# Performance work log

Hardware: AMD Instinct MI355X
Metric: run time of the kernel (lower is better)

## Reference

```python
import jax, jax.numpy as jnp
import numpy as np

N = 100000
E = 1600000
D_PCA = 50
D_BIO = 64
HID = 32
HEADS = 4
OUT = 50
EPS = 1e-5


def setup_inputs() -> dict:
    key = jax.random.key(0)
    ks = jax.random.split(key, 32)
    g = lambda i, shape, s=0.05: jax.random.normal(ks[i], shape, dtype=jnp.float32) * s
    inp = {
        'x_pca': jax.random.normal(ks[0], (N, D_PCA), dtype=jnp.float32),
        'x_bio': jax.random.normal(ks[1], (N, D_BIO), dtype=jnp.float32),
        'edge_index': jax.random.randint(ks[2], (2, E), 0, N, dtype=jnp.int32),
        # bio encoder: Linear(64,16) -> BN(16) -> ELU -> Linear(16,16) -> ELU
        'bioW1': g(3, (16, D_BIO)), 'biob1': g(4, (16,)),
        'bn0_g': 1.0 + g(5, (16,)), 'bn0_b': g(6, (16,)),
        'bn0_m': g(7, (16,)), 'bn0_v': 1.0 + 0.1 * jax.random.uniform(ks[8], (16,), dtype=jnp.float32),
        'bioW2': g(9, (16, 16)), 'biob2': g(10, (16,)),
        # GATv2 layer 1: in = 50+16 = 66, out = HEADS*HID concat
        'Wl1': g(11, (HEADS * HID, D_PCA + 16)), 'bl1': g(12, (HEADS * HID,)),
        'Wr1': g(13, (HEADS * HID, D_PCA + 16)), 'br1': g(14, (HEADS * HID,)),
        'att1': g(15, (HEADS, HID)), 'bias1': g(16, (HEADS * HID,)),
        'bn1_g': 1.0 + g(17, (HEADS * HID,)), 'bn1_b': g(18, (HEADS * HID,)),
        'bn1_m': g(19, (HEADS * HID,)), 'bn1_v': 1.0 + 0.1 * jax.random.uniform(ks[20], (HEADS * HID,), dtype=jnp.float32),
        # GATv2 layer 2: in = HEADS*HID, heads=1, concat=False
        'Wl2': g(21, (HID, HEADS * HID)), 'bl2': g(22, (HID,)),
        'Wr2': g(23, (HID, HEADS * HID)), 'br2': g(24, (HID,)),
        'att2': g(25, (1, HID)), 'bias2': g(26, (HID,)),
        'bn2_g': 1.0 + g(27, (HID,)), 'bn2_b': g(28, (HID,)),
        'bn2_m': g(29, (HID,)), 'bn2_v': 1.0 + 0.1 * jax.random.uniform(ks[30], (HID,), dtype=jnp.float32),
        'predW': g(31, (OUT, HID)), 'predb': jnp.zeros((OUT,), dtype=jnp.float32),
    }
    return inp


def _bn(h, gm, bt, mean, var):
    # BatchNorm1d in eval mode (running stats)
    return (h - mean) * jax.lax.rsqrt(var + EPS) * gm + bt


def _gatv2(x, src, dst, Wl, bl, Wr, br, att, bias, heads, out_dim, concat):
    n = x.shape[0]
    xl = (x @ Wl.T + bl).reshape(n, heads, out_dim)  # source transform
    xr = (x @ Wr.T + br).reshape(n, heads, out_dim)  # target transform
    e = jax.nn.leaky_relu(xl[src] + xr[dst], 0.2)    # [E,H,C]
    logits = jnp.einsum('ehc,hc->eh', e, att)        # [E,H]
    m = jax.ops.segment_max(logits, dst, num_segments=n)
    a = jnp.exp(logits - m[dst])
    denom = jax.ops.segment_sum(a, dst, num_segments=n)
    alpha = a / (denom[dst] + 1e-16)                 # segment softmax over dst
    out = jax.ops.segment_sum(xl[src] * alpha[..., None], dst, num_segments=n)
    out = out.reshape(n, heads * out_dim) if concat else out.mean(axis=1)
    return out + bias


def reference(x_pca, x_bio, edge_index,
              bioW1, biob1, bn0_g, bn0_b, bn0_m, bn0_v, bioW2, biob2,
              Wl1, bl1, Wr1, br1, att1, bias1, bn1_g, bn1_b, bn1_m, bn1_v,
              Wl2, bl2, Wr2, br2, att2, bias2, bn2_g, bn2_b, bn2_m, bn2_v,
              predW, predb):
    n = x_pca.shape[0]
    # add self-loops (PyG GATv2Conv default)
    loop = jnp.arange(n, dtype=edge_index.dtype)
    src = jnp.concatenate([edge_index[0], loop])
    dst = jnp.concatenate([edge_index[1], loop])

    # bio encoder
    h_bio = jax.nn.elu(_bn(x_bio @ bioW1.T + biob1, bn0_g, bn0_b, bn0_m, bn0_v))
    h_bio = jax.nn.elu(h_bio @ bioW2.T + biob2)
    x = jnp.concatenate([x_pca, h_bio], axis=1)  # [N, 66]

    h = _gatv2(x, src, dst, Wl1, bl1, Wr1, br1, att1, bias1, HEADS, HID, True)
    h = jax.nn.elu(_bn(h, bn1_g, bn1_b, bn1_m, bn1_v))  # dropout off (eval)
    h = _gatv2(h, src, dst, Wl2, bl2, Wr2, br2, att2, bias2, 1, HID, False)
    h = jax.nn.elu(_bn(h, bn2_g, bn2_b, bn2_m, bn2_v))
    return h @ predW.T + predb
```

## Files before the change

kernel.cpp:

```cpp
#include <hip/hip_runtime.h>
#include <hip/hip_fp16.h>
#include <cstdint>
#include <cstddef>

#define NN 100000
#define NE 1600000
#define NEP (NE + NN)
#define NBLK 200
#define CHUNK ((NEP + NBLK - 1) / NBLK)
#define NBUCK2 ((NN + 255) / 256)
#define HISTN (NBUCK2 * NBLK)
#define HSCAN_BLOCKS ((HISTN + 1023) / 1024)

typedef __attribute__((ext_vector_type(8))) _Float16 half8;
typedef __attribute__((ext_vector_type(4))) _Float16 h4v;
typedef __attribute__((ext_vector_type(2))) _Float16 h2v;
typedef __attribute__((ext_vector_type(4))) float float4v;

__device__ __forceinline__ float elu_f(float x) {
    return x > 0.f ? x : __expf(x) - 1.f;
}

__device__ __forceinline__ float ex2(float x) {
#if __has_builtin(__builtin_amdgcn_exp2f)
    return __builtin_amdgcn_exp2f(x);
#else
    return exp2f(x);
#endif
}

template<int CTRL>
__device__ __forceinline__ float dpp_add(float x) {
    int s = __builtin_amdgcn_update_dpp(0, __float_as_int(x), CTRL, 0xF, 0xF, true);
    return x + __int_as_float(s);
}
__device__ __forceinline__ float sum4_all(float x) {
    x = dpp_add<0xB1>(x); x = dpp_add<0x4E>(x);
    return x;
}
__device__ __forceinline__ float sum8_all(float x) {
    x = dpp_add<0xB1>(x); x = dpp_add<0x4E>(x); x = dpp_add<0x141>(x);
    return x;
}

__device__ __forceinline__ float dot2f(h2v a, h2v b, float c) {
#if __has_builtin(__builtin_amdgcn_fdot2)
    return __builtin_amdgcn_fdot2(a, b, c, false);
#else
    return fmaf((float)a[0], (float)b[0], fmaf((float)a[1], (float)b[1], c));
#endif
}

__device__ __forceinline__ h2v hmax2v(h2v a, h2v b) {
#if __has_builtin(__builtin_elementwise_max)
    return __builtin_elementwise_max(a, b);
#else
    __half2 r = __hmax2(*(__half2*)&a, *(__half2*)&b);
    return *(h2v*)&r;
#endif
}


__global__ __launch_bounds__(256) void part_hist(const int* __restrict__ ei, int* __restrict__ hist)
{
    __shared__ int cnt[NBUCK2];
    int tid = threadIdx.x, k = blockIdx.x;
    for (int i = tid; i < NBUCK2; i += 256) cnt[i] = 0;
    __syncthreads();
    int e0 = k * CHUNK, e1 = min(e0 + CHUNK, NEP);
    for (int e = e0 + tid; e < e1; e += 256) {
        int dst = (e < NE) ? ei[NE + e] : e - NE;
        atomicAdd(&cnt[dst >> 8], 1);
    }
    __syncthreads();
    for (int i = tid; i < NBUCK2; i += 256) hist[i * NBLK + k] = cnt[i];
}

__global__ __launch_bounds__(256) void scan_p1(const int* __restrict__ src, int* __restrict__ part, int n)
{
    __shared__ int wsum[4];
    int t = threadIdx.x;
    int i0 = blockIdx.x * 1024 + t * 4;
    int s = 0;
    if (i0 + 3 < n) { int4 d = *(const int4*)(src + i0); s = d.x + d.y + d.z + d.w; }
    else { for (int k = 0; k < 4; k++) if (i0 + k < n) s += src[i0 + k]; }
    for (int d = 1; d < 64; d <<= 1) s += __shfl_xor(s, d, 64);
    if ((t & 63) == 0) wsum[t >> 6] = s;
    __syncthreads();
    if (t == 0) part[blockIdx.x] = wsum[0] + wsum[1] + wsum[2] + wsum[3];
}

__global__ __launch_bounds__(128) void scan_p2(int* __restrict__ part, int nb, int* __restrict__ off)
{
    __shared__ int wt[2];
    int t = threadIdx.x;
    int lane = t & 63, w = t >> 6;
    int v = (t < nb) ? part[t] : 0;
    int x = v;
    for (int d = 1; d < 64; d <<= 1) { int y = __shfl_up(x, d, 64); if (lane >= d) x += y; }
    if (lane == 63) wt[w] = x;
    __syncthreads();
    int base = (w == 1) ? wt[0] : 0;
    int excl = base + x - v;
    if (t < nb) part[t] = excl;
    if (t == 0) off[NN] = NEP;
}

__global__ __launch_bounds__(256) void scan_p3(int* __restrict__ data, const int* __restrict__ part, int n)
{
    __shared__ int wsum[4];
    int t = threadIdx.x, lane = t & 63, w = t >> 6;
    int i0 = blockIdx.x * 1024 + t * 4;
    int d0 = 0, d1 = 0, d2 = 0, d3 = 0;
    if (i0 + 3 < n) { int4 d = *(const int4*)(data + i0); d0 = d.x; d1 = d.y; d2 = d.z; d3 = d.w; }
    else if (i0 < n) {
        d0 = data[i0];
        if (i0 + 1 < n) d1 = data[i0 + 1];
        if (i0 + 2 < n) d2 = data[i0 + 2];
    }
    int s = d0 + d1 + d2 + d3;
    int x = s;
    for (int d = 1; d < 64; d <<= 1) { int y = __shfl_up(x, d, 64); if (lane >= d) x += y; }
    if (lane == 63) wsum[w] = x;
    __syncthreads();
    int wb = 0;
    for (int i = 0; i < w; i++) wb += wsum[i];
    int base = part[blockIdx.x] + wb + x - s;
    if (i0 < n)     data[i0]     = base;
    if (i0 + 1 < n) data[i0 + 1] = base + d0;
    if (i0 + 2 < n) data[i0 + 2] = base + d0 + d1;
    if (i0 + 3 < n) data[i0 + 3] = base + d0 + d1 + d2;
}

__global__ __launch_bounds__(256) void part_scatter(const int* __restrict__ ei,
                                                    const int* __restrict__ hist,
                                                    unsigned* __restrict__ ebuf)
{
    __shared__ int cur[NBUCK2];
    int tid = threadIdx.x, k = blockIdx.x;
    for (int i = tid; i < NBUCK2; i += 256) cur[i] = hist[i * NBLK + k];
    __syncthreads();
    int e0 = k * CHUNK, e1 = min(e0 + CHUNK, NEP);
    for (int e = e0 + tid; e < e1; e += 256) {
        int src, dst;
        if (e < NE) { src = ei[e]; dst = ei[NE + e]; } else { src = dst = e - NE; }
        int pos = atomicAdd(&cur[dst >> 8], 1);
        ebuf[pos] = (unsigned)src | ((unsigned)(dst & 255) << 24);
    }
}

__global__ __launch_bounds__(256) void bucket_csr(const int* __restrict__ hist,
                                                  const unsigned* __restrict__ ebuf,
                                                  int* __restrict__ off, int* __restrict__ csr)
{
    __shared__ int cnt[256];
    __shared__ int cur[256];
    __shared__ int wsum[4];
    int b = blockIdx.x;
    int d0 = b << 8;
    int tid = threadIdx.x;
    int e0 = hist[b * NBLK];
    int e1 = (b + 1 < NBUCK2) ? hist[(b + 1) * NBLK] : NEP;
    cnt[tid] = 0;
    __syncthreads();
    for (int i = e0 + tid; i < e1; i += 256) atomicAdd(&cnt[ebuf[i] >> 24], 1);
    __syncthreads();
    int c = cnt[tid];
    int x = c;
    int lane = tid & 63, w = tid >> 6;
    for (int d = 1; d < 64; d <<= 1) { int y = __shfl_up(x, d, 64); if (lane >= d) x += y; }
    if (lane == 63) wsum[w] = x;
    __syncthreads();
    int wb = 0;
    for (int i = 0; i < w; i++) wb += wsum[i];
    int excl = wb + x - c;
    cur[tid] = e0 + excl;
    int node = d0 + tid;
    if (node < NN) off[node] = e0 + excl;
    __syncthreads();
    for (int i = e0 + tid; i < e1; i += 256) {
        unsigned v = ebuf[i];
        int p = atomicAdd(&cur[v >> 24], 1);
        csr[p] = (int)(v & 0xFFFFFF);
    }
}


__global__ __launch_bounds__(256) void bio_kernel(
    const float* __restrict__ xb, const float* __restrict__ xp,
    const float* __restrict__ W1, const float* __restrict__ b1,
    const float* __restrict__ g0, const float* __restrict__ bb0,
    const float* __restrict__ m0, const float* __restrict__ v0,
    const float* __restrict__ W2, const float* __restrict__ b2,
    __half* __restrict__ xh)
{
    __shared__ float sW1[16*64], sW2[16*16], sb1[16], sb2[16], ss[16], st[16];
    int tid = threadIdx.x;
    for (int idx = tid; idx < 1024; idx += 256) sW1[idx] = W1[idx];
    if (tid < 256) sW2[tid] = W2[tid];
    if (tid < 16) {
        sb1[tid] = b1[tid]; sb2[tid] = b2[tid];
        float s = g0[tid] * rsqrtf(v0[tid] + 1e-5f);
        ss[tid] = s; st[tid] = bb0[tid] - m0[tid] * s;
    }
    __syncthreads();
    int i = blockIdx.x * 256 + tid;
    if (i >= NN) return;
    float bio[64];
    const float4* p = (const float4*)(xb + (size_t)i * 64);
    #pragma unroll
    for (int q = 0; q < 16; q++) {
        float4 f = p[q];
        bio[q*4] = f.x; bio[q*4+1] = f.y; bio[q*4+2] = f.z; bio[q*4+3] = f.w;
    }
    float t1[16];
    #pragma unroll
    for (int j = 0; j < 16; j++) {
        float acc = sb1[j];
        #pragma unroll
        for (int k = 0; k < 64; k++) acc += bio[k] * sW1[j*64 + k];
        acc = acc * ss[j] + st[j];
        t1[j] = elu_f(acc);
    }
    __half* xrow = xh + (size_t)i * 96;
    const float* xpr = xp + (size_t)i * 50;
    #pragma unroll
    for (int j = 0; j < 25; j++) {
        float2 f = *(const float2*)(xpr + 2 * j);
        *(__half2*)(xrow + 2 * j) = __floats2half2_rn(f.x, f.y);
    }
    #pragma unroll
    for (int j = 0; j < 16; j++) {
        float acc = sb2[j];
        #pragma unroll
        for (int k = 0; k < 16; k++) acc += t1[k] * sW2[j*16 + k];
        xrow[50 + j] = __float2half(elu_f(acc));
    }
    __half2 z2 = __floats2half2_rn(0.f, 0.f);
    #pragma unroll
    for (int j = 0; j < 15; j++) *(__half2*)(xrow + 66 + 2 * j) = z2;
}


__global__ __launch_bounds__(256) void wconvert_all(
    const float* __restrict__ Wl1, const float* __restrict__ Wr1,
    const float* __restrict__ bl1, const float* __restrict__ br1,
    const float* __restrict__ Wl2, const float* __restrict__ Wr2,
    const float* __restrict__ bl2, const float* __restrict__ br2,
    const float* __restrict__ predW, const float* __restrict__ predb,
    const float* __restrict__ bias1, const float* __restrict__ bn1g,
    const float* __restrict__ bn1b, const float* __restrict__ bn1m,
    const float* __restrict__ bn1v,
    const float* __restrict__ bias2, const float* __restrict__ bn2g,
    const float* __restrict__ bn2b, const float* __restrict__ bn2m,
    const float* __restrict__ bn2v,
    __half* __restrict__ wcat1, float* __restrict__ bcat1,
    __half* __restrict__ wcat2, float* __restrict__ bcat2,
    __half* __restrict__ wpred, float* __restrict__ bpred,
    float* __restrict__ scb1, float* __restrict__ shb1,
    float* __restrict__ scb2, float* __restrict__ shb2)
{
    int t = blockIdx.x * 256 + threadIdx.x;
    if (t < 256 * 96) {
        int j = t / 96, k = t - j * 96;
        float v = (k < 66) ? ((j < 128) ? Wl1[j * 66 + k] : Wr1[(j - 128) * 66 + k]) : 0.f;
        wcat1[t] = __float2half(v);
    }
    int u = t - 256 * 96;
    if (u >= 0 && u < 64 * 128) {
        int j = u >> 7, k = u & 127;
        float v = (j < 32) ? Wl2[j * 128 + k] : Wr2[(j - 32) * 128 + k];
        wcat2[u] = __float2half(v);
    }
    int w = u - 64 * 128;
    if (w >= 0 && w < 64 * 32) {
        int j = w >> 5;
        wpred[w] = __float2half(j < 50 ? predW[w] : 0.f);
    }
    int z = w - 64 * 32;
    if (z >= 0 && z < 256) bcat1[z] = (z < 128) ? bl1[z] : br1[z - 128];
    int z2 = z - 256;
    if (z2 >= 0 && z2 < 64) bcat2[z2] = (z2 < 32) ? bl2[z2] : br2[z2 - 32];
    int z3 = z2 - 64;
    if (z3 >= 0 && z3 < 64) bpred[z3] = (z3 < 50) ? predb[z3] : 0.f;
    int z4 = z3 - 64;
    if (z4 >= 0 && z4 < 128) {
        float sc = bn1g[z4] * rsqrtf(bn1v[z4] + 1e-5f);
        scb1[z4] = sc;
        shb1[z4] = bn1b[z4] + (bias1[z4] - bn1m[z4]) * sc;
    }
    int z5 = z4 - 128;
    if (z5 >= 0 && z5 < 32) {
        float sc = bn2g[z5] * rsqrtf(bn2v[z5] + 1e-5f);
        scb2[z5] = sc;
        shb2[z5] = bn2b[z5] + (bias2[z5] - bn2m[z5]) * sc;
    }
}

template<int KT, int NC, int NCB, int NSPL, bool FOUT>
__global__ __launch_bounds__(256) void mfma_gemm(
    const __half* __restrict__ in, const __half* __restrict__ wcat,
    const float* __restrict__ bcat, void* __restrict__ outv, void* __restrict__ outv2,
    int n, int ncol)
{
    constexpr int K = KT * 32;
    constexpr int KP = K + 8;
    __shared__ __half sW[NCB * KP];
    __shared__ __half sX[64 * KP];
    __shared__ float sB[NCB];
    int tid = threadIdx.x;
    int co = blockIdx.y * NCB;
    for (int idx = tid * 8; idx < NCB * K; idx += 256 * 8) {
        int r = idx / K, c = idx - r * K;
        *(half8*)(&sW[r * KP + c]) = *(const half8*)(&wcat[(size_t)(co + r) * K + c]);
    }
    for (int idx = tid; idx < NCB; idx += 256) sB[idx] = bcat[co + idx];
    int row0 = blockIdx.x * 64;
    half8 hz = {0, 0, 0, 0, 0, 0, 0, 0};
    for (int idx = tid * 8; idx < 64 * K; idx += 256 * 8) {
        int r = idx / K, c = idx - r * K;
        int gr = row0 + r;
        half8 v = (gr < n) ? *(const half8*)(&in[(size_t)gr * K + c]) : hz;
        *(half8*)(&sX[r * KP + c]) = v;
    }
    __syncthreads();
    int w = tid >> 6, lane = tid & 63;
    int m = lane & 15, quad = lane >> 4;
    half8 a[KT];
    #pragma unroll
    for (int kt = 0; kt < KT; kt++)
        a[kt] = *(const half8*)(&sX[(w * 16 + m) * KP + kt * 32 + quad * 8]);
    #pragma unroll 1
    for (int nt = 0; nt < NCB / 16; nt++) {
        float4v acc = {0.f, 0.f, 0.f, 0.f};
        #pragma unroll
        for (int kt = 0; kt < KT; kt++) {
            half8 bfrag = *(const half8*)(&sW[(nt * 16 + m) * KP + kt * 32 + quad * 8]);
            acc = __builtin_amdgcn_mfma_f32_16x16x32_f16(a[kt], bfrag, acc, 0, 0, 0);
        }
        int col = co + nt * 16 + m;
        float bias = sB[nt * 16 + m];
        #pragma unroll
        for (int i = 0; i < 4; i++) {
            int r = row0 + w * 16 + quad * 4 + i;
            if (r < n) {
                if (FOUT) { if (col < ncol) ((float*)outv)[(size_t)r * ncol + col] = acc[i] + bias; }
                else if (col < NSPL)
                    ((__half*)outv)[(size_t)r * NSPL + col] = __float2half(acc[i] + bias);
                else
                    ((__half*)outv2)[(size_t)r * (NC - NSPL) + (col - NSPL)] = __float2half(acc[i] + bias);
            }
        }
    }
}

__global__ __launch_bounds__(256) void fused_gat1(
    const int* __restrict__ off, const int* __restrict__ csr,
    const __half* __restrict__ xl, const __half* __restrict__ xr,
    const float* __restrict__ att,
    const float* __restrict__ scb, const float* __restrict__ shb,
    __half* __restrict__ h1)
{
    int wave = threadIdx.x >> 6;
    int lane = threadIdx.x & 63;
    int node = blockIdx.x * 4 + wave;
    if (node >= NN) return;
    int row = lane >> 4;
    int cl  = lane & 15;
    int ch  = cl * 8;
    unsigned chb = (unsigned)cl * 16u;
    const char* xbase = (const char*)xl;
    const float LOG2E = 1.44269504088896f;

    half8 xr8 = *(const half8*)((const char*)xr + (size_t)node * 256 + chb);
    float4 af0 = *(const float4*)(att + ch);
    float4 af1 = *(const float4*)(att + ch + 4);
    h2v a01 = {(_Float16)(af0.x * LOG2E), (_Float16)(af0.y * LOG2E)};
    h2v a23 = {(_Float16)(af0.z * LOG2E), (_Float16)(af0.w * LOG2E)};
    h2v a45 = {(_Float16)(af1.x * LOG2E), (_Float16)(af1.y * LOG2E)};
    h2v a67 = {(_Float16)(af1.z * LOG2E), (_Float16)(af1.w * LOG2E)};
    h2v xr01 = {xr8[0], xr8[1]}, xr23 = {xr8[2], xr8[3]};
    h2v xr45 = {xr8[4], xr8[5]}, xr67 = {xr8[6], xr8[7]};
    const h2v c2 = {(_Float16)0.2f, (_Float16)0.2f};

    int k0 = off[node], k1 = off[node + 1];
    float acc0 = 0.f, acc1 = 0.f, acc2 = 0.f, acc3 = 0.f;
    float acc4 = 0.f, acc5 = 0.f, acc6 = 0.f, acc7 = 0.f, denom = 0.f;

    int rowp4  = row + 4;
    int rowp8  = row + 8;
    int rowp12 = row + 12;

    auto edge = [&](half8 cur, bool valid) {
        h2v xl01 = {cur[0], cur[1]}, xl23 = {cur[2], cur[3]};
        h2v xl45 = {cur[4], cur[5]}, xl67 = {cur[6], cur[7]};
        h2v s01 = xl01 + xr01, s23 = xl23 + xr23;
        h2v s45 = xl45 + xr45, s67 = xl67 + xr67;
        h2v l01 = hmax2v(s01, s01 * c2);
        h2v l23 = hmax2v(s23, s23 * c2);
        h2v l45 = hmax2v(s45, s45 * c2);
        h2v l67 = hmax2v(s67, s67 * c2);
        float pp = dot2f(l01, a01, dot2f(l23, a23, dot2f(l45, a45, dot2f(l67, a67, 0.f))));
        pp = sum4_all(pp);
        float wgt = valid ? ex2(pp) : 0.f;
        denom += wgt;
        acc0 = fmaf((float)cur[0], wgt, acc0);
        acc1 = fmaf((float)cur[1], wgt, acc1);
        acc2 = fmaf((float)cur[2], wgt, acc2);
        acc3 = fmaf((float)cur[3], wgt, acc3);
        acc4 = fmaf((float)cur[4], wgt, acc4);
        acc5 = fmaf((float)cur[5], wgt, acc5);
        acc6 = fmaf((float)cur[6], wgt, acc6);
        acc7 = fmaf((float)cur[7], wgt, acc7);
    };

    for (int base = k0; base < k1; base += 64) {
        int nb = min(64, k1 - base);
        int mysrc = (lane < nb) ? csr[base + lane] : 0;
        int i0 = __shfl(mysrc, row, 64);
        int i1 = __shfl(mysrc, rowp4, 64);
        half8 c0 = *(const half8*)(xbase + (((unsigned)i0 << 8) + chb));
        half8 c1 = *(const half8*)(xbase + (((unsigned)i1 << 8) + chb));
        #pragma unroll 2
        for (int t = 0; t < nb; t += 8) {
            int i2 = __shfl(mysrc, t + rowp8, 64);
            int i3 = __shfl(mysrc, t + rowp12, 64);
            half8 cc2 = *(const half8*)(xbase + (((unsigned)i2 << 8) + chb));
            half8 cc3 = *(const half8*)(xbase + (((unsigned)i3 << 8) + chb));
            edge(c0, (t + row) < nb);
            edge(c1, (t + rowp4) < nb);
            c0 = cc2; c1 = cc3;
        }
    }
    acc0 += __shfl_xor(acc0, 16, 64); acc0 += __shfl_xor(acc0, 32, 64);
    acc1 += __shfl_xor(acc1, 16, 64); acc1 += __shfl_xor(acc1, 32, 64);
    acc2 += __shfl_xor(acc2, 16, 64); acc2 += __shfl_xor(acc2, 32, 64);
    acc3 += __shfl_xor(acc3, 16, 64); acc3 += __shfl_xor(acc3, 32, 64);
    acc4 += __shfl_xor(acc4, 16, 64); acc4 += __shfl_xor(acc4, 32, 64);
    acc5 += __shfl_xor(acc5, 16, 64); acc5 += __shfl_xor(acc5, 32, 64);
    acc6 += __shfl_xor(acc6, 16, 64); acc6 += __shfl_xor(acc6, 32, 64);
    acc7 += __shfl_xor(acc7, 16, 64); acc7 += __shfl_xor(acc7, 32, 64);
    denom += __shfl_xor(denom, 16, 64); denom += __shfl_xor(denom, 32, 64);
    if (row == 0) {
        float inv = 1.f / (denom + 1e-16f);
        float4 s0 = *(const float4*)(scb + ch), s1 = *(const float4*)(scb + ch + 4);
        float4 h0 = *(const float4*)(shb + ch), h1f = *(const float4*)(shb + ch + 4);
        float o[8];
        o[0] = elu_f(fmaf(acc0 * inv, s0.x, h0.x));
        o[1] = elu_f(fmaf(acc1 * inv, s0.y, h0.y));
        o[2] = elu_f(fmaf(acc2 * inv, s0.z, h0.z));
        o[3] = elu_f(fmaf(acc3 * inv, s0.w, h0.w));
        o[4] = elu_f(fmaf(acc4 * inv, s1.x, h1f.x));
        o[5] = elu_f(fmaf(acc5 * inv, s1.y, h1f.y));
        o[6] = elu_f(fmaf(acc6 * inv, s1.z, h1f.z));
        o[7] = elu_f(fmaf(acc7 * inv, s1.w, h1f.w));
        half8 oh = {(_Float16)o[0], (_Float16)o[1], (_Float16)o[2], (_Float16)o[3],
                    (_Float16)o[4], (_Float16)o[5], (_Float16)o[6], (_Float16)o[7]};
        *(half8*)(h1 + (size_t)node * 128 + ch) = oh;
    }
}

__global__ __launch_bounds__(256) void fused_gat2(
    const int* __restrict__ off, const int* __restrict__ csr,
    const __half* __restrict__ xl2, const __half* __restrict__ xr2,
    const float* __restrict__ att,
    const float* __restrict__ scb, const float* __restrict__ shb,
    __half* __restrict__ h2)
{
    int wave = threadIdx.x >> 6;
    int lane = threadIdx.x & 63;
    int node = blockIdx.x * 4 + wave;
    if (node >= NN) return;
    int row = lane >> 3;
    int cl  = lane & 7;
    int ch  = cl * 4;
    unsigned chb = (unsigned)cl * 8u;
    const char* xbase = (const char*)xl2;
    const float LOG2E = 1.44269504088896f;

    h4v xr4 = *(const h4v*)((const char*)xr2 + (size_t)node * 64 + chb);
    h2v xr01 = {xr4[0], xr4[1]}, xr23 = {xr4[2], xr4[3]};
    float4 af = *(const float4*)(att + ch);
    h2v a01 = {(_Float16)(af.x * LOG2E), (_Float16)(af.y * LOG2E)};
    h2v a23 = {(_Float16)(af.z * LOG2E), (_Float16)(af.w * LOG2E)};
    const h2v c2 = {(_Float16)0.2f, (_Float16)0.2f};

    int k0 = off[node], k1 = off[node + 1];
    float acc0 = 0.f, acc1 = 0.f, acc2 = 0.f, acc3 = 0.f, denom = 0.f;

    int rowp8  = row + 8;
    int rowp16 = row + 16;
    int rowp24 = row + 24;

    auto edge = [&](h4v cur, bool valid) {
        h2v xl01 = {cur[0], cur[1]}, xl23 = {cur[2], cur[3]};
        h2v s01 = xl01 + xr01, s23 = xl23 + xr23;
        h2v l01 = hmax2v(s01, s01 * c2);
        h2v l23 = hmax2v(s23, s23 * c2);
        float pp = dot2f(l01, a01, dot2f(l23, a23, 0.f));
        pp = sum8_all(pp);
        float wgt = valid ? ex2(pp) : 0.f;
        denom += wgt;
        acc0 = fmaf((float)cur[0], wgt, acc0);
        acc1 = fmaf((float)cur[1], wgt, acc1);
        acc2 = fmaf((float)cur[2], wgt, acc2);
        acc3 = fmaf((float)cur[3], wgt, acc3);
    };

    for (int base = k0; base < k1; base += 64) {
        int nb = min(64, k1 - base);
        int mysrc = (lane < nb) ? csr[base + lane] : 0;
        int i0 = __shfl(mysrc, row, 64);
        int i1 = __shfl(mysrc, rowp8, 64);
        h4v c0 = *(const h4v*)(xbase + (((unsigned)i0 << 6) + chb));
        h4v c1 = *(const h4v*)(xbase + (((unsigned)i1 << 6) + chb));
        #pragma unroll 2
        for (int t = 0; t < nb; t += 16) {
            int i2 = __shfl(mysrc, t + rowp16, 64);
            int i3 = __shfl(mysrc, t + rowp24, 64);
            h4v cc2 = *(const h4v*)(xbase + (((unsigned)i2 << 6) + chb));
            h4v cc3 = *(const h4v*)(xbase + (((unsigned)i3 << 6) + chb));
            edge(c0, (t + row) < nb);
            edge(c1, (t + rowp8) < nb);
            c0 = cc2; c1 = cc3;
        }
    }
    acc0 += __shfl_xor(acc0, 8, 64); acc0 += __shfl_xor(acc0, 16, 64); acc0 += __shfl_xor(acc0, 32, 64);
    acc1 += __shfl_xor(acc1, 8, 64); acc1 += __shfl_xor(acc1, 16, 64); acc1 += __shfl_xor(acc1, 32, 64);
    acc2 += __shfl_xor(acc2, 8, 64); acc2 += __shfl_xor(acc2, 16, 64); acc2 += __shfl_xor(acc2, 32, 64);
    acc3 += __shfl_xor(acc3, 8, 64); acc3 += __shfl_xor(acc3, 16, 64); acc3 += __shfl_xor(acc3, 32, 64);
    denom += __shfl_xor(denom, 8, 64); denom += __shfl_xor(denom, 16, 64); denom += __shfl_xor(denom, 32, 64);
    if (row == 0) {
        float inv = 1.f / (denom + 1e-16f);
        float4 sv = *(const float4*)(scb + ch);
        float4 hv = *(const float4*)(shb + ch);
        float o0 = elu_f(fmaf(acc0 * inv, sv.x, hv.x));
        float o1 = elu_f(fmaf(acc1 * inv, sv.y, hv.y));
        float o2 = elu_f(fmaf(acc2 * inv, sv.z, hv.z));
        float o3 = elu_f(fmaf(acc3 * inv, sv.w, hv.w));
        h4v oh = {(_Float16)o0, (_Float16)o1, (_Float16)o2, (_Float16)o3};
        *(h4v*)(h2 + (size_t)node * 32 + ch) = oh;
    }
}

extern "C" void kernel_launch(void* const* d_in, const int* in_sizes, int n_in,
                              void* d_out, int out_size, void* d_ws, size_t ws_size,
                              hipStream_t stream)
{
    const float* x_pca = (const float*)d_in[0];
    const float* x_bio = (const float*)d_in[1];
    const int*   ei    = (const int*)d_in[2];
    const float* bioW1 = (const float*)d_in[3];
    const float* biob1 = (const float*)d_in[4];
    const float* bn0_g = (const float*)d_in[5];
    const float* bn0_b = (const float*)d_in[6];
    const float* bn0_m = (const float*)d_in[7];
    const float* bn0_v = (const float*)d_in[8];
    const float* bioW2 = (const float*)d_in[9];
    const float* biob2 = (const float*)d_in[10];
    const float* Wl1   = (const float*)d_in[11];
    const float* bl1   = (const float*)d_in[12];
    const float* Wr1   = (const float*)d_in[13];
    const float* br1   = (const float*)d_in[14];
    const float* att1  = (const float*)d_in[15];
    const float* bias1 = (const float*)d_in[16];
    const float* bn1_g = (const float*)d_in[17];
    const float* bn1_b = (const float*)d_in[18];
    const float* bn1_m = (const float*)d_in[19];
    const float* bn1_v = (const float*)d_in[20];
    const float* Wl2   = (const float*)d_in[21];
    const float* bl2   = (const float*)d_in[22];
    const float* Wr2   = (const float*)d_in[23];
    const float* br2   = (const float*)d_in[24];
    const float* att2  = (const float*)d_in[25];
    const float* bias2 = (const float*)d_in[26];
    const float* bn2_g = (const float*)d_in[27];
    const float* bn2_b = (const float*)d_in[28];
    const float* bn2_m = (const float*)d_in[29];
    const float* bn2_v = (const float*)d_in[30];
    const float* predW = (const float*)d_in[31];
    const float* predb = (const float*)d_in[32];

    __half* xh   = (__half*)d_ws;
    __half* xl1  = xh  + (size_t)NN * 96;
    __half* xr1  = xl1 + (size_t)NN * 128;
    __half* h1h  = xr1 + (size_t)NN * 128;
    __half* xl2  = h1h + (size_t)NN * 128;
    __half* xr2  = xl2 + (size_t)NN * 32;
    __half* h2h  = xr2 + (size_t)NN * 32;
    float*  p4   = (float*)(h2h + (size_t)NN * 32);
    __half* wcat1 = (__half*)p4;
    float*  bcat1 = p4 + 12288;
    __half* wcat2 = (__half*)(bcat1 + 256);
    float*  bcat2 = bcat1 + 256 + 4096;
    __half* wpred = (__half*)(bcat2 + 64);
    float*  bpred = bcat2 + 64 + 1024;
    float*  scb1  = bpred + 64;
    float*  shb1  = scb1 + 128;
    float*  scb2  = shb1 + 128;
    float*  shb2  = scb2 + 32;
    int*    ib    = (int*)(shb2 + 32);
    unsigned* ebuf = (unsigned*)ib;
    int*    hist   = ib + NEP;
    int*    part   = hist + HISTN;
    int*    off    = part + 128;
    int*    csr    = off + NN + 1;

    float* out = (float*)d_out;

    part_hist<<<NBLK, 256, 0, stream>>>(ei, hist);
    scan_p1<<<HSCAN_BLOCKS, 256, 0, stream>>>(hist, part, HISTN);
    scan_p2<<<1, 128, 0, stream>>>(part, HSCAN_BLOCKS, off);
    scan_p3<<<HSCAN_BLOCKS, 256, 0, stream>>>(hist, part, HISTN);
    part_scatter<<<NBLK, 256, 0, stream>>>(ei, hist, ebuf);
    bucket_csr<<<NBUCK2, 256, 0, stream>>>(hist, ebuf, off, csr);

    bio_kernel<<<(NN + 255) / 256, 256, 0, stream>>>(
        x_bio, x_pca, bioW1, biob1, bn0_g, bn0_b, bn0_m, bn0_v, bioW2, biob2, xh);

    wconvert_all<<<139, 256, 0, stream>>>(
        Wl1, Wr1, bl1, br1, Wl2, Wr2, bl2, br2, predW, predb,
        bias1, bn1_g, bn1_b, bn1_m, bn1_v,
        bias2, bn2_g, bn2_b, bn2_m, bn2_v,
        wcat1, bcat1, wcat2, bcat2, wpred, bpred,
        scb1, shb1, scb2, shb2);

    mfma_gemm<3, 256, 128, 128, false><<<dim3((NN + 63) / 64, 2), 256, 0, stream>>>(
        xh, wcat1, bcat1, xl1, xr1, NN, 0);

    fused_gat1<<<(NN + 3) / 4, 256, 0, stream>>>(
        off, csr, xl1, xr1, att1, scb1, shb1, h1h);

    mfma_gemm<4, 64, 64, 32, false><<<dim3((NN + 63) / 64, 1), 256, 0, stream>>>(
        h1h, wcat2, bcat2, xl2, xr2, NN, 0);

    fused_gat2<<<(NN + 3) / 4, 256, 0, stream>>>(
        off, csr, xl2, xr2, att2, scb2, shb2, h2h);

    mfma_gemm<1, 64, 64, 64, true><<<dim3((NN + 63) / 64, 1), 256, 0, stream>>>(
        h2h, wpred, bpred, out, nullptr, NN, 50);
}
```

Before: 393.0 us.

## Fuse prediction head into GAT2, process two nodes per wave, merge prep kernels

Merges the bio encoder and weight-conversion kernels into one launch split by block index. Fuses the final prediction linear layer into the second GAT aggregation kernel using shuffles and packed fp16 dot products, removing the intermediate h2 buffer and a GEMM launch. Each wave now processes two destination nodes at once to overlap more gathers, at the cost of more registers and divergence when the two degrees differ.

```diff
diff --git a/kernel.cpp b/kernel.cpp
--- a/kernel.cpp
+++ b/kernel.cpp
@@ -186,63 +186,13 @@
 }
 
 
-__global__ __launch_bounds__(256) void bio_kernel(
+__global__ __launch_bounds__(256) void bio_wconv(
     const float* __restrict__ xb, const float* __restrict__ xp,
     const float* __restrict__ W1, const float* __restrict__ b1,
     const float* __restrict__ g0, const float* __restrict__ bb0,
     const float* __restrict__ m0, const float* __restrict__ v0,
     const float* __restrict__ W2, const float* __restrict__ b2,
-    __half* __restrict__ xh)
-{
-    __shared__ float sW1[16*64], sW2[16*16], sb1[16], sb2[16], ss[16], st[16];
-    int tid = threadIdx.x;
-    for (int idx = tid; idx < 1024; idx += 256) sW1[idx] = W1[idx];
-    if (tid < 256) sW2[tid] = W2[tid];
-    if (tid < 16) {
-        sb1[tid] = b1[tid]; sb2[tid] = b2[tid];
-        float s = g0[tid] * rsqrtf(v0[tid] + 1e-5f);
-        ss[tid] = s; st[tid] = bb0[tid] - m0[tid] * s;
-    }
-    __syncthreads();
-    int i = blockIdx.x * 256 + tid;
-    if (i >= NN) return;
-    float bio[64];
-    const float4* p = (const float4*)(xb + (size_t)i * 64);
-    #pragma unroll
-    for (int q = 0; q < 16; q++) {
-        float4 f = p[q];
-        bio[q*4] = f.x; bio[q*4+1] = f.y; bio[q*4+2] = f.z; bio[q*4+3] = f.w;
-    }
-    float t1[16];
-    #pragma unroll
-    for (int j = 0; j < 16; j++) {
-        float acc = sb1[j];
-        #pragma unroll
-        for (int k = 0; k < 64; k++) acc += bio[k] * sW1[j*64 + k];
-        acc = acc * ss[j] + st[j];
-        t1[j] = elu_f(acc);
-    }
-    __half* xrow = xh + (size_t)i * 96;
-    const float* xpr = xp + (size_t)i * 50;
-    #pragma unroll
-    for (int j = 0; j < 25; j++) {
-        float2 f = *(const float2*)(xpr + 2 * j);
-        *(__half2*)(xrow + 2 * j) = __floats2half2_rn(f.x, f.y);
-    }
-    #pragma unroll
-    for (int j = 0; j < 16; j++) {
-        float acc = sb2[j];
-        #pragma unroll
-        for (int k = 0; k < 16; k++) acc += t1[k] * sW2[j*16 + k];
-        xrow[50 + j] = __float2half(elu_f(acc));
-    }
-    __half2 z2 = __floats2half2_rn(0.f, 0.f);
-    #pragma unroll
-    for (int j = 0; j < 15; j++) *(__half2*)(xrow + 66 + 2 * j) = z2;
-}
-
-
-__global__ __launch_bounds__(256) void wconvert_all(
+    __half* __restrict__ xh,
     const float* __restrict__ Wl1, const float* __restrict__ Wr1,
     const float* __restrict__ bl1, const float* __restrict__ br1,
     const float* __restrict__ Wl2, const float* __restrict__ Wr2,
@@ -260,40 +210,88 @@
     float* __restrict__ scb1, float* __restrict__ shb1,
     float* __restrict__ scb2, float* __restrict__ shb2)
 {
-    int t = blockIdx.x * 256 + threadIdx.x;
-    if (t < 256 * 96) {
-        int j = t / 96, k = t - j * 96;
-        float v = (k < 66) ? ((j < 128) ? Wl1[j * 66 + k] : Wr1[(j - 128) * 66 + k]) : 0.f;
-        wcat1[t] = __float2half(v);
-    }
-    int u = t - 256 * 96;
-    if (u >= 0 && u < 64 * 128) {
-        int j = u >> 7, k = u & 127;
-        float v = (j < 32) ? Wl2[j * 128 + k] : Wr2[(j - 32) * 128 + k];
-        wcat2[u] = __float2half(v);
-    }
-    int w = u - 64 * 128;
-    if (w >= 0 && w < 64 * 32) {
-        int j = w >> 5;
-        wpred[w] = __float2half(j < 50 ? predW[w] : 0.f);
-    }
-    int z = w - 64 * 32;
-    if (z >= 0 && z < 256) bcat1[z] = (z < 128) ? bl1[z] : br1[z - 128];
-    int z2 = z - 256;
-    if (z2 >= 0 && z2 < 64) bcat2[z2] = (z2 < 32) ? bl2[z2] : br2[z2 - 32];
-    int z3 = z2 - 64;
-    if (z3 >= 0 && z3 < 64) bpred[z3] = (z3 < 50) ? predb[z3] : 0.f;
-    int z4 = z3 - 64;
-    if (z4 >= 0 && z4 < 128) {
-        float sc = bn1g[z4] * rsqrtf(bn1v[z4] + 1e-5f);
-        scb1[z4] = sc;
-        shb1[z4] = bn1b[z4] + (bias1[z4] - bn1m[z4]) * sc;
-    }
-    int z5 = z4 - 128;
-    if (z5 >= 0 && z5 < 32) {
-        float sc = bn2g[z5] * rsqrtf(bn2v[z5] + 1e-5f);
-        scb2[z5] = sc;
-        shb2[z5] = bn2b[z5] + (bias2[z5] - bn2m[z5]) * sc;
+    __shared__ float sW1[16*64], sW2[16*16], sb1[16], sb2[16], ss[16], st[16];
+    int tid = threadIdx.x;
+    if (blockIdx.x < NBUCK2) {
+        for (int idx = tid; idx < 1024; idx += 256) sW1[idx] = W1[idx];
+        if (tid < 256) sW2[tid] = W2[tid];
+        if (tid < 16) {
+            sb1[tid] = b1[tid]; sb2[tid] = b2[tid];
+            float s = g0[tid] * rsqrtf(v0[tid] + 1e-5f);
+            ss[tid] = s; st[tid] = bb0[tid] - m0[tid] * s;
+        }
+        __syncthreads();
+        int i = blockIdx.x * 256 + tid;
+        if (i >= NN) return;
+        float bio[64];
+        const float4* p = (const float4*)(xb + (size_t)i * 64);
+        #pragma unroll
+        for (int q = 0; q < 16; q++) {
+            float4 f = p[q];
+            bio[q*4] = f.x; bio[q*4+1] = f.y; bio[q*4+2] = f.z; bio[q*4+3] = f.w;
+        }
+        float t1[16];
+        #pragma unroll
+        for (int j = 0; j < 16; j++) {
+            float acc = sb1[j];
+            #pragma unroll
+            for (int k = 0; k < 64; k++) acc += bio[k] * sW1[j*64 + k];
+            acc = acc * ss[j] + st[j];
+            t1[j] = elu_f(acc);
+        }
+        __half* xrow = xh + (size_t)i * 96;
+        const float* xpr = xp + (size_t)i * 50;
+        #pragma unroll
+        for (int j = 0; j < 25; j++) {
+            float2 f = *(const float2*)(xpr + 2 * j);
+            *(__half2*)(xrow + 2 * j) = __floats2half2_rn(f.x, f.y);
+        }
+        #pragma unroll
+        for (int j = 0; j < 16; j++) {
+            float acc = sb2[j];
+            #pragma unroll
+            for (int k = 0; k < 16; k++) acc += t1[k] * sW2[j*16 + k];
+            xrow[50 + j] = __float2half(elu_f(acc));
+        }
+        __half2 z2 = __floats2half2_rn(0.f, 0.f);
+        #pragma unroll
+        for (int j = 0; j < 15; j++) *(__half2*)(xrow + 66 + 2 * j) = z2;
+    } else {
+        int t = (blockIdx.x - NBUCK2) * 256 + tid;
+        if (t < 256 * 96) {
+            int j = t / 96, k = t - j * 96;
+            float v = (k < 66) ? ((j < 128) ? Wl1[j * 66 + k] : Wr1[(j - 128) * 66 + k]) : 0.f;
+            wcat1[t] = __float2half(v);
+        }
+        int u = t - 256 * 96;
+        if (u >= 0 && u < 64 * 128) {
+            int j = u >> 7, k = u & 127;
+            float v = (j < 32) ? Wl2[j * 128 + k] : Wr2[(j - 32) * 128 + k];
+            wcat2[u] = __float2half(v);
+        }
+        int w = u - 64 * 128;
+        if (w >= 0 && w < 64 * 32) {
+            int j = w >> 5;
+            wpred[w] = __float2half(j < 50 ? predW[w] : 0.f);
+        }
+        int z = w - 64 * 32;
+        if (z >= 0 && z < 256) bcat1[z] = (z < 128) ? bl1[z] : br1[z - 128];
+        int z2 = z - 256;
+        if (z2 >= 0 && z2 < 64) bcat2[z2] = (z2 < 32) ? bl2[z2] : br2[z2 - 32];
+        int z3 = z2 - 64;
+        if (z3 >= 0 && z3 < 64) bpred[z3] = (z3 < 50) ? predb[z3] : 0.f;
+        int z4 = z3 - 64;
+        if (z4 >= 0 && z4 < 128) {
+            float sc = bn1g[z4] * rsqrtf(bn1v[z4] + 1e-5f);
+            scb1[z4] = sc;
+            shb1[z4] = bn1b[z4] + (bias1[z4] - bn1m[z4]) * sc;
+        }
+        int z5 = z4 - 128;
+        if (z5 >= 0 && z5 < 32) {
+            float sc = bn2g[z5] * rsqrtf(bn2v[z5] + 1e-5f);
+            scb2[z5] = sc;
+            shb2[z5] = bn2b[z5] + (bias2[z5] - bn2m[z5]) * sc;
+        }
     }
 }
 
@@ -460,17 +458,78 @@
     }
 }
 
+struct Acc2 { float a0,a1,a2,a3,dn; };
+
+__device__ __forceinline__ void edge2(
+    Acc2& s, h4v cur, bool valid,
+    h2v xr01, h2v xr23, h2v a01, h2v a23, h2v c2)
+{
+    h2v xl01 = {cur[0], cur[1]}, xl23 = {cur[2], cur[3]};
+    h2v s01 = xl01 + xr01, s23 = xl23 + xr23;
+    h2v l01 = hmax2v(s01, s01 * c2);
+    h2v l23 = hmax2v(s23, s23 * c2);
+    float pp = dot2f(l01, a01, dot2f(l23, a23, 0.f));
+    pp = sum8_all(pp);
+    float wgt = valid ? ex2(pp) : 0.f;
+    s.dn += wgt;
+    s.a0 = fmaf((float)cur[0], wgt, s.a0);
+    s.a1 = fmaf((float)cur[1], wgt, s.a1);
+    s.a2 = fmaf((float)cur[2], wgt, s.a2);
+    s.a3 = fmaf((float)cur[3], wgt, s.a3);
+}
+
+__device__ __forceinline__ h4v finish2v(
+    Acc2& s, int ch,
+    const float* __restrict__ scb, const float* __restrict__ shb)
+{
+    s.a0 += __shfl_xor(s.a0, 8, 64); s.a0 += __shfl_xor(s.a0, 16, 64); s.a0 += __shfl_xor(s.a0, 32, 64);
+    s.a1 += __shfl_xor(s.a1, 8, 64); s.a1 += __shfl_xor(s.a1, 16, 64); s.a1 += __shfl_xor(s.a1, 32, 64);
+    s.a2 += __shfl_xor(s.a2, 8, 64); s.a2 += __shfl_xor(s.a2, 16, 64); s.a2 += __shfl_xor(s.a2, 32, 64);
+    s.a3 += __shfl_xor(s.a3, 8, 64); s.a3 += __shfl_xor(s.a3, 16, 64); s.a3 += __shfl_xor(s.a3, 32, 64);
+    s.dn += __shfl_xor(s.dn, 8, 64); s.dn += __shfl_xor(s.dn, 16, 64); s.dn += __shfl_xor(s.dn, 32, 64);
+    float inv = 1.f / (s.dn + 1e-16f);
+    float4 sv = *(const float4*)(scb + ch);
+    float4 hv = *(const float4*)(shb + ch);
+    float o0 = elu_f(fmaf(s.a0 * inv, sv.x, hv.x));
+    float o1 = elu_f(fmaf(s.a1 * inv, sv.y, hv.y));
+    float o2 = elu_f(fmaf(s.a2 * inv, sv.z, hv.z));
+    float o3 = elu_f(fmaf(s.a3 * inv, sv.w, hv.w));
+    h4v oh = {(_Float16)o0, (_Float16)o1, (_Float16)o2, (_Float16)o3};
+    return oh;
+}
+
+__device__ __forceinline__ void predstore(
+    h4v oh, int node, int lane,
+    half8 w0, half8 w1, half8 w2, half8 w3,
+    float bp, float* __restrict__ out)
+{
+    int2 u = *(int2*)&oh;
+    float acc = 0.f;
+#define PREDK(k, wv, r) { int b0 = __shfl(u.x, k, 64); int b1 = __shfl(u.y, k, 64); \
+    h2v h01 = *(h2v*)&b0, h23 = *(h2v*)&b1; \
+    h2v w01 = {wv[r], wv[r+1]}, w23 = {wv[r+2], wv[r+3]}; \
+    acc = dot2f(h01, w01, acc); acc = dot2f(h23, w23, acc); }
+    PREDK(0, w0, 0) PREDK(1, w0, 4)
+    PREDK(2, w1, 0) PREDK(3, w1, 4)
+    PREDK(4, w2, 0) PREDK(5, w2, 4)
+    PREDK(6, w3, 0) PREDK(7, w3, 4)
+#undef PREDK
+    if (lane < 50) out[(size_t)node * 50 + lane] = acc + bp;
+}
+
 __global__ __launch_bounds__(256) void fused_gat2(
     const int* __restrict__ off, const int* __restrict__ csr,
     const __half* __restrict__ xl2, const __half* __restrict__ xr2,
     const float* __restrict__ att,
     const float* __restrict__ scb, const float* __restrict__ shb,
-    __half* __restrict__ h2)
+    const __half* __restrict__ wpred, const float* __restrict__ bpred,
+    float* __restrict__ out)
 {
     int wave = threadIdx.x >> 6;
     int lane = threadIdx.x & 63;
-    int node = blockIdx.x * 4 + wave;
-    if (node >= NN) return;
+    int nA = blockIdx.x * 8 + wave * 2;
+    int nB = nA + 1;
+    if (nA >= NN) return;
     int row = lane >> 3;
     int cl  = lane & 7;
     int ch  = cl * 4;
@@ -478,69 +537,68 @@
     const char* xbase = (const char*)xl2;
     const float LOG2E = 1.44269504088896f;
 
-    h4v xr4 = *(const h4v*)((const char*)xr2 + (size_t)node * 64 + chb);
-    h2v xr01 = {xr4[0], xr4[1]}, xr23 = {xr4[2], xr4[3]};
+    h4v xrA4 = *(const h4v*)((const char*)xr2 + (size_t)nA * 64 + chb);
+    h4v xrB4 = *(const h4v*)((const char*)xr2 + (size_t)nB * 64 + chb);
+    h2v xA01 = {xrA4[0], xrA4[1]}, xA23 = {xrA4[2], xrA4[3]};
+    h2v xB01 = {xrB4[0], xrB4[1]}, xB23 = {xrB4[2], xrB4[3]};
     float4 af = *(const float4*)(att + ch);
     h2v a01 = {(_Float16)(af.x * LOG2E), (_Float16)(af.y * LOG2E)};
     h2v a23 = {(_Float16)(af.z * LOG2E), (_Float16)(af.w * LOG2E)};
     const h2v c2 = {(_Float16)0.2f, (_Float16)0.2f};
 
-    int k0 = off[node], k1 = off[node + 1];
-    float acc0 = 0.f, acc1 = 0.f, acc2 = 0.f, acc3 = 0.f, denom = 0.f;
+    const __half* wrow = wpred + lane * 32;
+    half8 w0 = *(const half8*)(wrow);
+    half8 w1 = *(const half8*)(wrow + 8);
+    half8 w2 = *(const half8*)(wrow + 16);
+    half8 w3 = *(const half8*)(wrow + 24);
+    float bp = (lane < 50) ? bpred[lane] : 0.f;
+
+    int baseA = off[nA];
+    int kA1   = off[nA + 1];
+    int baseB = kA1;
+    int kB1   = off[nA + 2];
+
+    Acc2 sA = {0.f,0.f,0.f,0.f,0.f};
+    Acc2 sB = {0.f,0.f,0.f,0.f,0.f};
 
     int rowp8  = row + 8;
     int rowp16 = row + 16;
     int rowp24 = row + 24;
 
-    auto edge = [&](h4v cur, bool valid) {
-        h2v xl01 = {cur[0], cur[1]}, xl23 = {cur[2], cur[3]};
-        h2v s01 = xl01 + xr01, s23 = xl23 + xr23;
-        h2v l01 = hmax2v(s01, s01 * c2);
-        h2v l23 = hmax2v(s23, s23 * c2);
-        float pp = dot2f(l01, a01, dot2f(l23, a23, 0.f));
-        pp = sum8_all(pp);
-        float wgt = valid ? ex2(pp) : 0.f;
-        denom += wgt;
-        acc0 = fmaf((float)cur[0], wgt, acc0);
-        acc1 = fmaf((float)cur[1], wgt, acc1);
-        acc2 = fmaf((float)cur[2], wgt, acc2);
-        acc3 = fmaf((float)cur[3], wgt, acc3);
-    };
-
-    for (int base = k0; base < k1; base += 64) {
-        int nb = min(64, k1 - base);
-        int mysrc = (lane < nb) ? csr[base + lane] : 0;
-        int i0 = __shfl(mysrc, row, 64);
-        int i1 = __shfl(mysrc, rowp8, 64);
-        h4v c0 = *(const h4v*)(xbase + (((unsigned)i0 << 6) + chb));
-        h4v c1 = *(const h4v*)(xbase + (((unsigned)i1 << 6) + chb));
-        #pragma unroll 2
-        for (int t = 0; t < nb; t += 16) {
-            int i2 = __shfl(mysrc, t + rowp16, 64);
-            int i3 = __shfl(mysrc, t + rowp24, 64);
-            h4v cc2 = *(const h4v*)(xbase + (((unsigned)i2 << 6) + chb));
-            h4v cc3 = *(const h4v*)(xbase + (((unsigned)i3 << 6) + chb));
-            edge(c0, (t + row) < nb);
-            edge(c1, (t + rowp8) < nb);
-            c0 = cc2; c1 = cc3;
-        }
-    }
-    acc0 += __shfl_xor(acc0, 8, 64); acc0 += __shfl_xor(acc0, 16, 64); acc0 += __shfl_xor(acc0, 32, 64);
-    acc1 += __shfl_xor(acc1, 8, 64); acc1 += __shfl_xor(acc1, 16, 64); acc1 += __shfl_xor(acc1, 32, 64);
-    acc2 += __shfl_xor(acc2, 8, 64); acc2 += __shfl_xor(acc2, 16, 64); acc2 += __shfl_xor(acc2, 32, 64);
-    acc3 += __shfl_xor(acc3, 8, 64); acc3 += __shfl_xor(acc3, 16, 64); acc3 += __shfl_xor(acc3, 32, 64);
-    denom += __shfl_xor(denom, 8, 64); denom += __shfl_xor(denom, 16, 64); denom += __shfl_xor(denom, 32, 64);
-    if (row == 0) {
-        float inv = 1.f / (denom + 1e-16f);
-        float4 sv = *(const float4*)(scb + ch);
-        float4 hv = *(const float4*)(shb + ch);
-        float o0 = elu_f(fmaf(acc0 * inv, sv.x, hv.x));
-        float o1 = elu_f(fmaf(acc1 * inv, sv.y, hv.y));
-        float o2 = elu_f(fmaf(acc2 * inv, sv.z, hv.z));
-        float o3 = elu_f(fmaf(acc3 * inv, sv.w, hv.w));
-        h4v oh = {(_Float16)o0, (_Float16)o1, (_Float16)o2, (_Float16)o3};
-        *(h4v*)(h2 + (size_t)node * 32 + ch) = oh;
-    }
+    while (baseA < kA1 || baseB < kB1) {
+        int remA = kA1 - baseA, remB = kB1 - baseB;
+        int nbA = remA > 0 ? min(64, remA) : 0;
+        int nbB = remB > 0 ? min(64, remB) : 0;
+        int srcA = (lane < nbA) ? csr[baseA + lane] : 0;
+        int srcB = (lane < nbB) ? csr[baseB + lane] : 0;
+        int nt = max(nbA, nbB);
+        int iA0 = __shfl(srcA, row, 64),   iA1 = __shfl(srcA, rowp8, 64);
+        int iB0 = __shfl(srcB, row, 64),   iB1 = __shfl(srcB, rowp8, 64);
+        h4v cA0 = *(const h4v*)(xbase + (((unsigned)iA0 << 6) + chb));
+        h4v cA1 = *(const h4v*)(xbase + (((unsigned)iA1 << 6) + chb));
+        h4v cB0 = *(const h4v*)(xbase + (((unsigned)iB0 << 6) + chb));
+        h4v cB1 = *(const h4v*)(xbase + (((unsigned)iB1 << 6) + chb));
+        for (int t = 0; t < nt; t += 16) {
+            int jA0 = __shfl(srcA, t + rowp16, 64);
+            int jA1 = __shfl(srcA, t + rowp24, 64);
+            int jB0 = __shfl(srcB, t + rowp16, 64);
+            int jB1 = __shfl(srcB, t + rowp24, 64);
+            h4v pA0 = *(const h4v*)(xbase + (((unsigned)jA0 << 6) + chb));
+            h4v pA1 = *(const h4v*)(xbase + (((unsigned)jA1 << 6) + chb));
+            h4v pB0 = *(const h4v*)(xbase + (((unsigned)jB0 << 6) + chb));
+            h4v pB1 = *(const h4v*)(xbase + (((unsigned)jB1 << 6) + chb));
+            edge2(sA, cA0, (t + row)   < nbA, xA01, xA23, a01, a23, c2);
+            edge2(sA, cA1, (t + rowp8) < nbA, xA01, xA23, a01, a23, c2);
+            edge2(sB, cB0, (t + row)   < nbB, xB01, xB23, a01, a23, c2);
+            edge2(sB, cB1, (t + rowp8) < nbB, xB01, xB23, a01, a23, c2);
+            cA0 = pA0; cA1 = pA1; cB0 = pB0; cB1 = pB1;
+        }
+        baseA += 64; baseB += 64;
+    }
+    h4v ohA = finish2v(sA, ch, scb, shb);
+    h4v ohB = finish2v(sB, ch, scb, shb);
+    predstore(ohA, nA, lane, w0, w1, w2, w3, bp, out);
+    predstore(ohB, nB, lane, w0, w1, w2, w3, bp, out);
 }
 
 extern "C" void kernel_launch(void* const* d_in, const int* in_sizes, int n_in,
@@ -587,8 +645,7 @@
     __half* h1h  = xr1 + (size_t)NN * 128;
     __half* xl2  = h1h + (size_t)NN * 128;
     __half* xr2  = xl2 + (size_t)NN * 32;
-    __half* h2h  = xr2 + (size_t)NN * 32;
-    float*  p4   = (float*)(h2h + (size_t)NN * 32);
+    float*  p4   = (float*)(xr2 + (size_t)NN * 32);
     __half* wcat1 = (__half*)p4;
     float*  bcat1 = p4 + 12288;
     __half* wcat2 = (__half*)(bcat1 + 256);
@@ -615,10 +672,8 @@
     part_scatter<<<NBLK, 256, 0, stream>>>(ei, hist, ebuf);
     bucket_csr<<<NBUCK2, 256, 0, stream>>>(hist, ebuf, off, csr);
 
-    bio_kernel<<<(NN + 255) / 256, 256, 0, stream>>>(
-        x_bio, x_pca, bioW1, biob1, bn0_g, bn0_b, bn0_m, bn0_v, bioW2, biob2, xh);
-
-    wconvert_all<<<139, 256, 0, stream>>>(
+    bio_wconv<<<NBUCK2 + 139, 256, 0, stream>>>(
+        x_bio, x_pca, bioW1, biob1, bn0_g, bn0_b, bn0_m, bn0_v, bioW2, biob2, xh,
         Wl1, Wr1, bl1, br1, Wl2, Wr2, bl2, br2, predW, predb,
         bias1, bn1_g, bn1_b, bn1_m, bn1_v,
         bias2, bn2_g, bn2_b, bn2_m, bn2_v,
@@ -634,9 +689,6 @@
     mfma_gemm<4, 64, 64, 32, false><<<dim3((NN + 63) / 64, 1), 256, 0, stream>>>(
         h1h, wcat2, bcat2, xl2, xr2, NN, 0);
 
-    fused_gat2<<<(NN + 3) / 4, 256, 0, stream>>>(
-        off, csr, xl2, xr2, att2, scb2, shb2, h2h);
-
-    mfma_gemm<1, 64, 64, 64, true><<<dim3((NN + 63) / 64, 1), 256, 0, stream>>>(
-        h2h, wpred, bpred, out, nullptr, NN, 50);
-}
+    fused_gat2<<<(NN + 7) / 8, 256, 0, stream>>>(
+        off, csr, xl2, xr2, att2, scb2, shb2, wpred, bpred, out);
+}
```

New measurement: 387.7 us. No clear change (-1.4%).
